# Kernel optimization log

Hardware: AMD Instinct MI355X
Metric: run time of the kernel (lower is better)

## Reference

```python
import jax, jax.numpy as jnp
import numpy as np

HIDDEN = 512
HEADS = 8


def setup_inputs() -> dict:
    key = jax.random.key(0)
    ks = jax.random.split(key, 7)
    B, S, D = 4, 2048, HIDDEN
    scale = 1.0 / np.sqrt(D)
    return {
        "src": jax.random.normal(ks[0], (B, S, D), dtype=jnp.float32),
        "Wq": jax.random.normal(ks[1], (D, D), dtype=jnp.float32) * scale,
        "bq": jax.random.normal(ks[2], (D,), dtype=jnp.float32) * 0.01,
        "Wk": jax.random.normal(ks[3], (D, D), dtype=jnp.float32) * scale,
        "bk": jax.random.normal(ks[4], (D,), dtype=jnp.float32) * 0.01,
        "Wv": jax.random.normal(ks[5], (D, D), dtype=jnp.float32) * scale,
        "bv": jax.random.normal(ks[6], (D,), dtype=jnp.float32) * 0.01,
    }


def reference(src, Wq, bq, Wk, bk, Wv, bv):
    B, S, D = src.shape
    H = HEADS
    hd = D // H
    # QKV projections -> [B, S, H, hd]
    q = (src @ Wq + bq).reshape(B, S, H, hd)
    k = (src @ Wk + bk).reshape(B, S, H, hd)
    v = (src @ Wv + bv).reshape(B, S, H, hd)
    # scores [B, H, S, S]; note: NO causal mask (matches original module)
    scores = jnp.einsum("bqhd,bkhd->bhqk", q, k) / jnp.sqrt(jnp.asarray(hd, src.dtype))
    attn = jax.nn.softmax(scores, axis=-1)
    out = jnp.einsum("bhqk,bkhd->bqhd", attn, v)
    return out.reshape(B, S, D)
```

## Files before the change

### kernel.cpp

```cpp
#include <hip/hip_runtime.h>

typedef __bf16 bf16;
typedef __bf16 bf16x8 __attribute__((ext_vector_type(8)));
typedef __bf16 bf16x4 __attribute__((ext_vector_type(4)));
typedef float f32x4 __attribute__((ext_vector_type(4)));
typedef float f32x16 __attribute__((ext_vector_type(16)));
typedef unsigned int u32;

#define QK_SCALE 0.1803368801111204f

__device__ __forceinline__ int rc16(int row, int g) {
    return row * 256 + ((g ^ (row & 15)) << 4);
}
__device__ __forceinline__ int swzb(int row, int col) {
    return (((row) << 7) + ((col) << 1)) ^ (((row) & 7) << 4);
}

__device__ __forceinline__ void gload_lds16(const void* g, void* l) {
    __builtin_amdgcn_global_load_lds(
        (const __attribute__((address_space(1))) unsigned int*)g,
        (__attribute__((address_space(3))) unsigned int*)l, 16, 0, 0);
}

__device__ __forceinline__ u32 cvtpk(float lo, float hi) {
    u32 r;
    asm("v_cvt_pk_bf16_f32 %0, %1, %2" : "=v"(r) : "v"(lo), "v"(hi));
    return r;
}
__device__ __forceinline__ void pl32swap(u32& a, u32& b) {
    asm("v_permlane32_swap_b32 %0, %1" : "+v"(a), "+v"(b));
}

__global__ __launch_bounds__(256) void cast_src(const float* __restrict__ x,
                                                bf16* __restrict__ y) {
    int i = blockIdx.x * 256 + threadIdx.x;
    float4 v = reinterpret_cast<const float4*>(x)[i];
    bf16x4 p;
    p[0] = (bf16)v.x; p[1] = (bf16)v.y; p[2] = (bf16)v.z; p[3] = (bf16)v.w;
    reinterpret_cast<bf16x4*>(y)[i] = p;
}

__global__ __launch_bounds__(256) void wtrans_all(const float* __restrict__ Wq,
                                                  const float* __restrict__ Wk,
                                                  const float* __restrict__ Wv,
                                                  bf16* __restrict__ Wt_all) {
    __shared__ float T[64][65];
    const int w = blockIdx.z;
    const float* W = w == 0 ? Wq : (w == 1 ? Wk : Wv);
    const float wsc = (w == 0) ? QK_SCALE : 1.0f;
    bf16* Wt = Wt_all + (size_t)w * 512 * 512;
    const int k0 = blockIdx.x * 64, n0 = blockIdx.y * 64;
    const int tx = threadIdx.x & 63, ty = threadIdx.x >> 6;
#pragma unroll
    for (int i = 0; i < 16; ++i) {
        int row = ty * 16 + i;
        T[row][tx] = W[(size_t)(k0 + row) * 512 + n0 + tx];
    }
    __syncthreads();
#pragma unroll
    for (int i = 0; i < 16; ++i) {
        int row = ty * 16 + i;
        Wt[(size_t)(n0 + row) * 512 + k0 + tx] = (bf16)(T[tx][row] * wsc);
    }
}

__global__ __launch_bounds__(256) void qkv_gemm_all(const bf16* __restrict__ srcb,
                                                    const bf16* __restrict__ Wt_all,
                                                    const float* __restrict__ bq,
                                                    const float* __restrict__ bk,
                                                    const float* __restrict__ bv,
                                                    bf16* __restrict__ Qb,
                                                    bf16* __restrict__ Kb,
                                                    bf16* __restrict__ Vtb) {
    __shared__ __align__(16) bf16 As[128 * 64];
    __shared__ __align__(16) bf16 Bs[128 * 64];
    const int t = threadIdx.x, lane = t & 63, wid = t >> 6;
    const int m0 = blockIdx.x * 128;
    const int n0g = blockIdx.y * 128;
    const int oi = n0g >> 9, n0 = n0g & 511;
    const float* bias = oi == 0 ? bq : (oi == 1 ? bk : bv);
    const float bsc = (oi == 0) ? QK_SCALE : 1.0f;
    bf16* outp = oi == 0 ? Qb : (oi == 1 ? Kb : Vtb);
    const bf16* Wt = Wt_all + (size_t)oi * 512 * 512;
    const bool sw = (oi == 2);
    const int wm = (wid >> 1) * 64, wn = (wid & 1) * 64;
    const int fr = lane & 15, fq = lane >> 4;

    f32x4 acc[4][4] = {};

    for (int k0 = 0; k0 < 512; k0 += 64) {
        __syncthreads();
#pragma unroll
        for (int c = 0; c < 4; ++c) {
            int u = (wid * 4 + c) * 64 + lane;
            int row = u >> 3;
            int slot = (u & 7) ^ (row & 7);
            gload_lds16(srcb + (size_t)(m0 + row) * 512 + k0 + slot * 8,
                        (char*)As + (wid * 4 + c) * 1024);
            gload_lds16(Wt + (size_t)(n0 + row) * 512 + k0 + slot * 8,
                        (char*)Bs + (wid * 4 + c) * 1024);
        }
        __syncthreads();

        bf16x8 a[2][4], b[2][4];
#pragma unroll
        for (int c = 0; c < 2; ++c)
#pragma unroll
            for (int i = 0; i < 4; ++i) {
                a[c][i] = *reinterpret_cast<const bf16x8*>(
                    (const char*)As + swzb(wm + i * 16 + fr, c * 32 + fq * 8));
                b[c][i] = *reinterpret_cast<const bf16x8*>(
                    (const char*)Bs + swzb(wn + i * 16 + fr, c * 32 + fq * 8));
            }
        if (!sw) {
#pragma unroll
            for (int i = 0; i < 4; ++i)
#pragma unroll
                for (int j = 0; j < 4; ++j)
#pragma unroll
                    for (int c = 0; c < 2; ++c)
                        acc[i][j] = __builtin_amdgcn_mfma_f32_16x16x32_bf16(a[c][i], b[c][j], acc[i][j], 0, 0, 0);
        } else {
#pragma unroll
            for (int i = 0; i < 4; ++i)
#pragma unroll
                for (int j = 0; j < 4; ++j)
#pragma unroll
                    for (int c = 0; c < 2; ++c)
                        acc[i][j] = __builtin_amdgcn_mfma_f32_16x16x32_bf16(b[c][j], a[c][i], acc[i][j], 0, 0, 0);
        }
    }

    if (!sw) {
#pragma unroll
        for (int j = 0; j < 4; ++j) {
            int n = n0 + wn + j * 16 + fr;
            float bj = bias[n] * bsc;
            int h = n >> 6, d = n & 63;
#pragma unroll
            for (int i = 0; i < 4; ++i)
#pragma unroll
                for (int r = 0; r < 4; ++r) {
                    int m = m0 + wm + i * 16 + fq * 4 + r;
                    int b_ = m >> 11, s = m & 2047;
                    outp[(((size_t)(b_ * 8 + h)) * 2048 + s) * 64 + d] =
                        (bf16)(acc[i][j][r] + bj);
                }
        }
    } else {
#pragma unroll
        for (int j = 0; j < 4; ++j)
#pragma unroll
            for (int r = 0; r < 4; ++r) {
                int n = n0 + wn + j * 16 + fq * 4 + r;
                float bj = bias[n];
                int h = n >> 6, d = n & 63;
#pragma unroll
                for (int i = 0; i < 4; ++i) {
                    int m = m0 + wm + i * 16 + fr;
                    int b_ = m >> 11, s = m & 2047;
                    outp[(((size_t)(b_ * 8 + h)) * 64 + d) * 2048 + s] =
                        (bf16)(acc[i][j][r] + bj);
                }
            }
    }
}

__global__ __launch_bounds__(512, 2) void attn_fwd(const bf16* __restrict__ Q,
                                                   const bf16* __restrict__ K,
                                                   const bf16* __restrict__ Vt,
                                                   float* __restrict__ out) {
    __shared__ __align__(16) char lds_raw[98304];
    const int t = threadIdx.x, lane = t & 63, wid = t >> 6;
    const int grp = wid >> 2, w4 = wid & 3;
    const int c31 = lane & 31, h = lane >> 5;
    const int bh = blockIdx.x & 31;
    const int qchunk = blockIdx.x >> 5;
    const int qw = qchunk * 256 + w4 * 64;

    bf16x8 qf0[4], qf1[4];
    {
        const bf16* Qp0 = Q + ((size_t)bh * 2048 + qw + c31) * 64;
        const bf16* Qp1 = Qp0 + 32 * 64;
#pragma unroll
        for (int ks = 0; ks < 4; ++ks) {
            qf0[ks] = *reinterpret_cast<const bf16x8*>(&Qp0[ks * 16 + h * 8]);
            qf1[ks] = *reinterpret_cast<const bf16x8*>(&Qp1[ks * 16 + h * 8]);
        }
    }

    bf16x8 bones;
#pragma unroll
    for (int e = 0; e < 8; ++e) bones[e] = (bf16)1.0f;

    f32x16 acc_o[2][2] = {};
    f32x16 acc_l[2] = {};

    const char* Kpb0 = (const char*)(K + (size_t)bh * 2048 * 64);
    const char* Vpb0 = (const char*)(Vt + (size_t)bh * 64 * 2048);

    auto stage = [&](int buf, int tt) {
        const size_t kv0 = (size_t)(grp * 1024 + tt * 64);
        const char* Kg = Kpb0 + kv0 * 128;
        const char* Vg = Vpb0 + kv0 * 2;
        char* Kl = lds_raw + (grp * 3 + buf) * 8192;
        char* Vl = lds_raw + 49152 + (grp * 3 + buf) * 8192;
#pragma unroll
        for (int c = 0; c < 2; ++c) {
            int ch = w4 * 2 + c;
            int r = ch * 4 + (lane >> 4);
            int g = (lane & 15) ^ (r & 15);
            gload_lds16(Kg + r * 256 + g * 16, Kl + ch * 1024);
            gload_lds16(Vg + (size_t)(2 * r + (g >> 3)) * 4096 + (g & 7) * 16,
                        Vl + ch * 1024);
        }
    };

    const int rq = c31 >> 1, gb = (c31 & 1) * 8;

    auto compute = [&](int buf) {
        const char* Kl = lds_raw + (grp * 3 + buf) * 8192;
        const char* Vl = lds_raw + 49152 + (grp * 3 + buf) * 8192;

        f32x16 s00 = {}, s01 = {}, s10 = {}, s11 = {};
        __builtin_amdgcn_s_setprio(1);
#pragma unroll
        for (int ks = 0; ks < 4; ++ks) {
            int g = gb + ks * 2 + h;
            bf16x8 kf0 = *reinterpret_cast<const bf16x8*>(Kl + rc16(rq, g));
            s00 = __builtin_amdgcn_mfma_f32_32x32x16_bf16(kf0, qf0[ks], s00, 0, 0, 0);
            s10 = __builtin_amdgcn_mfma_f32_32x32x16_bf16(kf0, qf1[ks], s10, 0, 0, 0);
            bf16x8 kf1 = *reinterpret_cast<const bf16x8*>(Kl + rc16(16 + rq, g));
            s01 = __builtin_amdgcn_mfma_f32_32x32x16_bf16(kf1, qf0[ks], s01, 0, 0, 0);
            s11 = __builtin_amdgcn_mfma_f32_32x32x16_bf16(kf1, qf1[ks], s11, 0, 0, 0);
        }
        __builtin_amdgcn_s_setprio(0);

        bf16x8 pa0[4], pa1[4];
#pragma unroll
        for (int st = 0; st < 2; ++st) {
            f32x16& sa = st ? s10 : s00;
            f32x16& sb = st ? s11 : s01;
#pragma unroll
            for (int r = 0; r < 16; ++r) {
                sa[r] = __builtin_amdgcn_exp2f(sa[r]);
                sb[r] = __builtin_amdgcn_exp2f(sb[r]);
            }
#pragma unroll
            for (int ktl = 0; ktl < 2; ++ktl) {
                const f32x16& sv = ktl ? sb : sa;
#pragma unroll
                for (int k2 = 0; k2 < 2; ++k2) {
                    u32 X = cvtpk(sv[8 * k2 + 0], sv[8 * k2 + 1]);
                    u32 Y = cvtpk(sv[8 * k2 + 4], sv[8 * k2 + 5]);
                    u32 Z = cvtpk(sv[8 * k2 + 2], sv[8 * k2 + 3]);
                    u32 W = cvtpk(sv[8 * k2 + 6], sv[8 * k2 + 7]);
                    pl32swap(X, Y);
                    pl32swap(Z, W);
                    union { bf16x8 v; u32 w[4]; } pu;
                    pu.w[0] = X; pu.w[1] = Z; pu.w[2] = Y; pu.w[3] = W;
                    if (st) pa1[ktl * 2 + k2] = pu.v;
                    else    pa0[ktl * 2 + k2] = pu.v;
                }
            }
        }

        __builtin_amdgcn_s_setprio(1);
#pragma unroll
        for (int kg = 0; kg < 4; ++kg) {
            int g = gb + kg * 2 + h;
            bf16x8 vf0 = *reinterpret_cast<const bf16x8*>(Vl + rc16(rq, g));
            acc_o[0][0] = __builtin_amdgcn_mfma_f32_32x32x16_bf16(pa0[kg], vf0, acc_o[0][0], 0, 0, 0);
            acc_o[1][0] = __builtin_amdgcn_mfma_f32_32x32x16_bf16(pa1[kg], vf0, acc_o[1][0], 0, 0, 0);
            bf16x8 vf1 = *reinterpret_cast<const bf16x8*>(Vl + rc16(16 + rq, g));
            acc_o[0][1] = __builtin_amdgcn_mfma_f32_32x32x16_bf16(pa0[kg], vf1, acc_o[0][1], 0, 0, 0);
            acc_o[1][1] = __builtin_amdgcn_mfma_f32_32x32x16_bf16(pa1[kg], vf1, acc_o[1][1], 0, 0, 0);
            acc_l[0] = __builtin_amdgcn_mfma_f32_32x32x16_bf16(pa0[kg], bones, acc_l[0], 0, 0, 0);
            acc_l[1] = __builtin_amdgcn_mfma_f32_32x32x16_bf16(pa1[kg], bones, acc_l[1], 0, 0, 0);
        }
        __builtin_amdgcn_s_setprio(0);
    };

    stage(0, 0);
    stage(1, 1);
    for (int tt = 0; tt < 16; ++tt) {
        if (tt < 15) {
            asm volatile("s_waitcnt vmcnt(4)" ::: "memory");
        } else {
            asm volatile("s_waitcnt vmcnt(0)" ::: "memory");
        }
        __builtin_amdgcn_s_barrier();
        if (tt + 2 < 16) stage((tt + 2) % 3, tt + 2);
        compute(tt % 3);
    }

    __syncthreads();

    float* Os = (float*)lds_raw;
    float* Ls = (float*)(lds_raw + 65536);
    if (grp == 1) {
#pragma unroll
        for (int st = 0; st < 2; ++st)
#pragma unroll
            for (int reg = 0; reg < 16; ++reg) {
                int qr = (reg & 3) + 8 * (reg >> 2) + 4 * h;
                int ql = w4 * 64 + st * 32 + qr;
                Os[ql * 64 + c31]      = acc_o[st][0][reg];
                Os[ql * 64 + 32 + c31] = acc_o[st][1][reg];
                if (c31 == 0) Ls[ql] = acc_l[st][reg];
            }
    }
    __syncthreads();
    if (grp == 0) {
        const int b_ = bh >> 3, hh = bh & 7;
#pragma unroll
        for (int st = 0; st < 2; ++st)
#pragma unroll
            for (int reg = 0; reg < 16; ++reg) {
                int qr = (reg & 3) + 8 * (reg >> 2) + 4 * h;
                int ql = w4 * 64 + st * 32 + qr;
                float l = acc_l[st][reg] + Ls[ql];
                float inv = __builtin_amdgcn_rcpf(l);
                int s_ = qchunk * 256 + ql;
                size_t base = ((size_t)b_ * 2048 + s_) * 512 + hh * 64;
                out[base + c31] =
                    (acc_o[st][0][reg] + Os[ql * 64 + c31]) * inv;
                out[base + 32 + c31] =
                    (acc_o[st][1][reg] + Os[ql * 64 + 32 + c31]) * inv;
            }
    }
}

extern "C" void kernel_launch(void* const* d_in, const int* in_sizes, int n_in,
                              void* d_out, int out_size, void* d_ws, size_t ws_size,
                              hipStream_t stream) {
    const float* src = (const float*)d_in[0];
    const float* Wq  = (const float*)d_in[1];
    const float* bq  = (const float*)d_in[2];
    const float* Wk  = (const float*)d_in[3];
    const float* bk  = (const float*)d_in[4];
    const float* Wv  = (const float*)d_in[5];
    const float* bv  = (const float*)d_in[6];
    float* out = (float*)d_out;

    char* ws = (char*)d_ws;
    const size_t WT_SZ  = 512u * 512u * sizeof(bf16);
    const size_t QKV_SZ = 8192u * 512u * sizeof(bf16);
    bf16* WtA  = (bf16*)(ws);
    bf16* srcb = (bf16*)(ws + 3 * WT_SZ);
    bf16* Qb   = (bf16*)(ws + 3 * WT_SZ + QKV_SZ);
    bf16* Kb   = (bf16*)(ws + 3 * WT_SZ + 2 * QKV_SZ);
    bf16* Vtb  = (bf16*)(ws + 3 * WT_SZ + 3 * QKV_SZ);

    cast_src<<<4096, 256, 0, stream>>>(src, srcb);
    wtrans_all<<<dim3(8, 8, 3), 256, 0, stream>>>(Wq, Wk, Wv, WtA);

    qkv_gemm_all<<<dim3(64, 12), 256, 0, stream>>>(srcb, WtA, bq, bk, bv, Qb, Kb, Vtb);

    attn_fwd<<<256, 512, 0, stream>>>(Qb, Kb, Vtb, out);
}
```

Measured before the change: 78.15 us.

## Load K/V fragments directly to registers and stage Q in LDS

Replaces the triple-buffered LDS staging of K and V tiles, with its barriers, by per-wave direct global loads of K and V fragments into registers, prefetching the next K tile during compute. Q is instead staged once per wave into LDS and reread for each score MFMA, which cuts resident Q registers and shrinks the LDS footprint. This removes block-wide barriers and LDS traffic for K/V. The cost is that the four waves sharing a group now each read the same K/V from global/L2 instead of sharing them, and global load latency is exposed with only one tile of lookahead.

```diff
diff --git a/kernel.cpp b/kernel.cpp
--- a/kernel.cpp
+++ b/kernel.cpp
@@ -170,7 +170,7 @@
                                                    const bf16* __restrict__ K,
                                                    const bf16* __restrict__ Vt,
                                                    float* __restrict__ out) {
-    __shared__ __align__(16) char lds_raw[98304];
+    __shared__ __align__(16) char lds_raw[66560];
     const int t = threadIdx.x, lane = t & 63, wid = t >> 6;
     const int grp = wid >> 2, w4 = wid & 3;
     const int c31 = lane & 31, h = lane >> 5;
@@ -178,16 +178,16 @@
     const int qchunk = blockIdx.x >> 5;
     const int qw = qchunk * 256 + w4 * 64;
 
-    bf16x8 qf0[4], qf1[4];
-    {
-        const bf16* Qp0 = Q + ((size_t)bh * 2048 + qw + c31) * 64;
-        const bf16* Qp1 = Qp0 + 32 * 64;
-#pragma unroll
-        for (int ks = 0; ks < 4; ++ks) {
-            qf0[ks] = *reinterpret_cast<const bf16x8*>(&Qp0[ks * 16 + h * 8]);
-            qf1[ks] = *reinterpret_cast<const bf16x8*>(&Qp1[ks * 16 + h * 8]);
-        }
-    }
+    char* Qlds = lds_raw + wid * 8192;
+    const char* Qg = (const char*)(Q + ((size_t)bh * 2048 + qw) * 64);
+#pragma unroll
+    for (int c = 0; c < 8; ++c) {
+        int r = c * 4 + (lane >> 4);
+        int g = (lane & 15) ^ (r & 15);
+        gload_lds16(Qg + r * 256 + g * 16, Qlds + c * 1024);
+    }
+    asm volatile("s_waitcnt vmcnt(0)" ::: "memory");
+    __builtin_amdgcn_sched_barrier(0);
 
     bf16x8 bones;
 #pragma unroll
@@ -198,100 +198,98 @@
 
     const char* Kpb0 = (const char*)(K + (size_t)bh * 2048 * 64);
     const char* Vpb0 = (const char*)(Vt + (size_t)bh * 64 * 2048);
-
-    auto stage = [&](int buf, int tt) {
-        const size_t kv0 = (size_t)(grp * 1024 + tt * 64);
-        const char* Kg = Kpb0 + kv0 * 128;
-        const char* Vg = Vpb0 + kv0 * 2;
-        char* Kl = lds_raw + (grp * 3 + buf) * 8192;
-        char* Vl = lds_raw + 49152 + (grp * 3 + buf) * 8192;
-#pragma unroll
-        for (int c = 0; c < 2; ++c) {
-            int ch = w4 * 2 + c;
-            int r = ch * 4 + (lane >> 4);
-            int g = (lane & 15) ^ (r & 15);
-            gload_lds16(Kg + r * 256 + g * 16, Kl + ch * 1024);
-            gload_lds16(Vg + (size_t)(2 * r + (g >> 3)) * 4096 + (g & 7) * 16,
-                        Vl + ch * 1024);
+    const int rq = c31 >> 1, gb = (c31 & 1) * 8;
+
+    bf16x8 k0[4], k1[4], v0[4], v1[4];
+
+    auto loadK = [&](int tt) {
+        const char* Kt = Kpb0 + (size_t)(grp * 1024 + tt * 64) * 128;
+#pragma unroll
+        for (int ks = 0; ks < 4; ++ks) {
+            k0[ks] = *reinterpret_cast<const bf16x8*>(Kt + c31 * 128 + (ks * 2 + h) * 16);
+            k1[ks] = *reinterpret_cast<const bf16x8*>(Kt + (32 + c31) * 128 + (ks * 2 + h) * 16);
         }
     };
-
-    const int rq = c31 >> 1, gb = (c31 & 1) * 8;
-
-    auto compute = [&](int buf) {
-        const char* Kl = lds_raw + (grp * 3 + buf) * 8192;
-        const char* Vl = lds_raw + 49152 + (grp * 3 + buf) * 8192;
-
-        f32x16 s00 = {}, s01 = {}, s10 = {}, s11 = {};
+    auto loadV = [&](int tt) {
+        const char* Vg = Vpb0 + (size_t)(grp * 1024 + tt * 64) * 2;
+#pragma unroll
+        for (int kg = 0; kg < 4; ++kg) {
+            v0[kg] = *reinterpret_cast<const bf16x8*>(Vg + (size_t)c31 * 4096 + (kg * 2 + h) * 16);
+            v1[kg] = *reinterpret_cast<const bf16x8*>(Vg + (size_t)(32 + c31) * 4096 + (kg * 2 + h) * 16);
+        }
+    };
+
+    auto mkpa = [&](const f32x16& sa, const f32x16& sb, bf16x8 pa[4]) {
+#pragma unroll
+        for (int ktl = 0; ktl < 2; ++ktl) {
+            const f32x16& sv = ktl ? sb : sa;
+#pragma unroll
+            for (int k2 = 0; k2 < 2; ++k2) {
+                u32 X = cvtpk(sv[8 * k2 + 0], sv[8 * k2 + 1]);
+                u32 Y = cvtpk(sv[8 * k2 + 4], sv[8 * k2 + 5]);
+                u32 Z = cvtpk(sv[8 * k2 + 2], sv[8 * k2 + 3]);
+                u32 W = cvtpk(sv[8 * k2 + 6], sv[8 * k2 + 7]);
+                pl32swap(X, Y);
+                pl32swap(Z, W);
+                union { bf16x8 v; u32 w[4]; } pu;
+                pu.w[0] = X; pu.w[1] = Z; pu.w[2] = Y; pu.w[3] = W;
+                pa[ktl * 2 + k2] = pu.v;
+            }
+        }
+    };
+
+    loadK(0);
+
+    for (int tt = 0; tt < 16; ++tt) {
+        loadV(tt);
+
+        f32x16 s0 = {}, s1 = {};
         __builtin_amdgcn_s_setprio(1);
 #pragma unroll
         for (int ks = 0; ks < 4; ++ks) {
-            int g = gb + ks * 2 + h;
-            bf16x8 kf0 = *reinterpret_cast<const bf16x8*>(Kl + rc16(rq, g));
-            s00 = __builtin_amdgcn_mfma_f32_32x32x16_bf16(kf0, qf0[ks], s00, 0, 0, 0);
-            s10 = __builtin_amdgcn_mfma_f32_32x32x16_bf16(kf0, qf1[ks], s10, 0, 0, 0);
-            bf16x8 kf1 = *reinterpret_cast<const bf16x8*>(Kl + rc16(16 + rq, g));
-            s01 = __builtin_amdgcn_mfma_f32_32x32x16_bf16(kf1, qf0[ks], s01, 0, 0, 0);
-            s11 = __builtin_amdgcn_mfma_f32_32x32x16_bf16(kf1, qf1[ks], s11, 0, 0, 0);
+            bf16x8 qf = *reinterpret_cast<const bf16x8*>(Qlds + rc16(rq, gb + ks * 2 + h));
+            s0 = __builtin_amdgcn_mfma_f32_32x32x16_bf16(k0[ks], qf, s0, 0, 0, 0);
+            s1 = __builtin_amdgcn_mfma_f32_32x32x16_bf16(k1[ks], qf, s1, 0, 0, 0);
         }
         __builtin_amdgcn_s_setprio(0);
-
-        bf16x8 pa0[4], pa1[4];
-#pragma unroll
-        for (int st = 0; st < 2; ++st) {
-            f32x16& sa = st ? s10 : s00;
-            f32x16& sb = st ? s11 : s01;
-#pragma unroll
-            for (int r = 0; r < 16; ++r) {
-                sa[r] = __builtin_amdgcn_exp2f(sa[r]);
-                sb[r] = __builtin_amdgcn_exp2f(sb[r]);
-            }
-#pragma unroll
-            for (int ktl = 0; ktl < 2; ++ktl) {
-                const f32x16& sv = ktl ? sb : sa;
-#pragma unroll
-                for (int k2 = 0; k2 < 2; ++k2) {
-                    u32 X = cvtpk(sv[8 * k2 + 0], sv[8 * k2 + 1]);
-                    u32 Y = cvtpk(sv[8 * k2 + 4], sv[8 * k2 + 5]);
-                    u32 Z = cvtpk(sv[8 * k2 + 2], sv[8 * k2 + 3]);
-                    u32 W = cvtpk(sv[8 * k2 + 6], sv[8 * k2 + 7]);
-                    pl32swap(X, Y);
-                    pl32swap(Z, W);
-                    union { bf16x8 v; u32 w[4]; } pu;
-                    pu.w[0] = X; pu.w[1] = Z; pu.w[2] = Y; pu.w[3] = W;
-                    if (st) pa1[ktl * 2 + k2] = pu.v;
-                    else    pa0[ktl * 2 + k2] = pu.v;
-                }
-            }
-        }
-
+        bf16x8 pa0[4];
+#pragma unroll
+        for (int r = 0; r < 16; ++r) {
+            s0[r] = __builtin_amdgcn_exp2f(s0[r]);
+            s1[r] = __builtin_amdgcn_exp2f(s1[r]);
+        }
+        mkpa(s0, s1, pa0);
+
+        f32x16 s2 = {}, s3 = {};
         __builtin_amdgcn_s_setprio(1);
 #pragma unroll
+        for (int ks = 0; ks < 4; ++ks) {
+            bf16x8 qf = *reinterpret_cast<const bf16x8*>(Qlds + rc16(16 + rq, gb + ks * 2 + h));
+            s2 = __builtin_amdgcn_mfma_f32_32x32x16_bf16(k0[ks], qf, s2, 0, 0, 0);
+            s3 = __builtin_amdgcn_mfma_f32_32x32x16_bf16(k1[ks], qf, s3, 0, 0, 0);
+        }
+        __builtin_amdgcn_s_setprio(0);
+        bf16x8 pa1[4];
+#pragma unroll
+        for (int r = 0; r < 16; ++r) {
+            s2[r] = __builtin_amdgcn_exp2f(s2[r]);
+            s3[r] = __builtin_amdgcn_exp2f(s3[r]);
+        }
+        mkpa(s2, s3, pa1);
+
+        if (tt < 15) loadK(tt + 1);
+
+        __builtin_amdgcn_s_setprio(1);
+#pragma unroll
         for (int kg = 0; kg < 4; ++kg) {
-            int g = gb + kg * 2 + h;
-            bf16x8 vf0 = *reinterpret_cast<const bf16x8*>(Vl + rc16(rq, g));
-            acc_o[0][0] = __builtin_amdgcn_mfma_f32_32x32x16_bf16(pa0[kg], vf0, acc_o[0][0], 0, 0, 0);
-            acc_o[1][0] = __builtin_amdgcn_mfma_f32_32x32x16_bf16(pa1[kg], vf0, acc_o[1][0], 0, 0, 0);
-            bf16x8 vf1 = *reinterpret_cast<const bf16x8*>(Vl + rc16(16 + rq, g));
-            acc_o[0][1] = __builtin_amdgcn_mfma_f32_32x32x16_bf16(pa0[kg], vf1, acc_o[0][1], 0, 0, 0);
-            acc_o[1][1] = __builtin_amdgcn_mfma_f32_32x32x16_bf16(pa1[kg], vf1, acc_o[1][1], 0, 0, 0);
+            acc_o[0][0] = __builtin_amdgcn_mfma_f32_32x32x16_bf16(pa0[kg], v0[kg], acc_o[0][0], 0, 0, 0);
+            acc_o[1][0] = __builtin_amdgcn_mfma_f32_32x32x16_bf16(pa1[kg], v0[kg], acc_o[1][0], 0, 0, 0);
+            acc_o[0][1] = __builtin_amdgcn_mfma_f32_32x32x16_bf16(pa0[kg], v1[kg], acc_o[0][1], 0, 0, 0);
+            acc_o[1][1] = __builtin_amdgcn_mfma_f32_32x32x16_bf16(pa1[kg], v1[kg], acc_o[1][1], 0, 0, 0);
             acc_l[0] = __builtin_amdgcn_mfma_f32_32x32x16_bf16(pa0[kg], bones, acc_l[0], 0, 0, 0);
             acc_l[1] = __builtin_amdgcn_mfma_f32_32x32x16_bf16(pa1[kg], bones, acc_l[1], 0, 0, 0);
         }
         __builtin_amdgcn_s_setprio(0);
-    };
-
-    stage(0, 0);
-    stage(1, 1);
-    for (int tt = 0; tt < 16; ++tt) {
-        if (tt < 15) {
-            asm volatile("s_waitcnt vmcnt(4)" ::: "memory");
-        } else {
-            asm volatile("s_waitcnt vmcnt(0)" ::: "memory");
-        }
-        __builtin_amdgcn_s_barrier();
-        if (tt + 2 < 16) stage((tt + 2) % 3, tt + 2);
-        compute(tt % 3);
     }
 
     __syncthreads();
```

After: 103.0 us. +31.8%, slower.
